# Kernel optimization log

Measured on AMD Instinct MI355X. Metric: run time of the kernel, lower is better.

Reference implementation:

```python
import jax, jax.numpy as jnp
import numpy as np

D_MODEL = 256
D_STATE = 256
BATCH = 32
SEQ = 4096
RMIN, RMAX = 0.9, 0.999
NEG_SLOPE = 0.01
EPS = 1e-5


def layer_norm(x, w=None, b=None):
    m = jnp.mean(x, axis=-1, keepdims=True)
    v = jnp.var(x, axis=-1, keepdims=True)
    y = (x - m) * jax.lax.rsqrt(v + EPS)
    if w is not None:
        y = y * w + b
    return y


def leaky_relu(x):
    return jnp.where(x >= 0, x, NEG_SLOPE * x)


def setup_inputs() -> dict:
    key = jax.random.key(0)
    ks = jax.random.split(key, 12)
    x = jax.random.normal(ks[0], (BATCH, SEQ, D_MODEL), dtype=jnp.float32)
    # LRU ring init: |lambda| uniform in [rmin, rmax], phase uniform in [0, 2pi]
    u1 = jax.random.uniform(ks[1], (D_STATE,), dtype=jnp.float32)
    u2 = jax.random.uniform(ks[2], (D_STATE,), dtype=jnp.float32)
    nu_log = jnp.log(-0.5 * jnp.log(u1 * (RMAX**2 - RMIN**2) + RMIN**2))
    theta_log = jnp.log(2 * jnp.pi * u2)
    lam_mod = jnp.exp(-jnp.exp(nu_log))
    gamma_log = jnp.log(jnp.sqrt(1.0 - lam_mod**2))
    B_re = jax.random.normal(ks[3], (D_STATE, D_MODEL)) / np.sqrt(2 * D_MODEL)
    B_im = jax.random.normal(ks[4], (D_STATE, D_MODEL)) / np.sqrt(2 * D_MODEL)
    C_re = jax.random.normal(ks[5], (D_STATE, D_STATE)) / np.sqrt(D_STATE)
    C_im = jax.random.normal(ks[6], (D_STATE, D_STATE)) / np.sqrt(D_STATE)
    Dm = jax.random.normal(ks[7], (D_STATE, D_MODEL)) / np.sqrt(D_MODEL)
    Wl = jax.random.normal(ks[8], (D_MODEL, D_STATE)) / np.sqrt(D_STATE)
    bl = jax.random.normal(ks[9], (D_MODEL,)) * 0.02
    Wr = jax.random.normal(ks[10], (D_MODEL, D_STATE)) / np.sqrt(D_STATE)
    br = jax.random.normal(ks[11], (D_MODEL,)) * 0.02
    ones_m = jnp.ones((D_MODEL,), jnp.float32)
    zeros_m = jnp.zeros((D_MODEL,), jnp.float32)
    ones_s = jnp.ones((D_STATE,), jnp.float32)
    zeros_s = jnp.zeros((D_STATE,), jnp.float32)
    return {
        "x": x,
        "ln1_w": ones_m, "ln1_b": zeros_m,
        "nu_log": nu_log, "theta_log": theta_log, "gamma_log": gamma_log,
        "B_re": B_re, "B_im": B_im, "C_re": C_re, "C_im": C_im, "Dm": Dm,
        "ln2_w": ones_s, "ln2_b": zeros_s,
        "Wl": Wl, "bl": bl, "Wr": Wr, "br": br,
        "ln4_w": ones_m, "ln4_b": zeros_m,
    }


def reference(x, ln1_w, ln1_b, nu_log, theta_log, gamma_log, B_re, B_im,
              C_re, C_im, Dm, ln2_w, ln2_b, Wl, bl, Wr, br, ln4_w, ln4_b):
    # pre-norm + residual skip
    x1 = layer_norm(x, ln1_w, ln1_b)          # [B, T, d_model]
    skip = x1
    u = leaky_relu(x1)
    # LRU: h_t = lambda * h_{t-1} + gamma * (B u_t); y = Re(C h) + D u
    lam_mod = jnp.exp(-jnp.exp(nu_log))
    theta = jnp.exp(theta_log)
    lr = lam_mod * jnp.cos(theta)             # [N]
    li = lam_mod * jnp.sin(theta)
    gam = jnp.exp(gamma_log)
    bu_re = gam * jnp.einsum('btd,nd->btn', u, B_re)  # [B, T, N]
    bu_im = gam * jnp.einsum('btd,nd->btn', u, B_im)
    bu_re_t = jnp.swapaxes(bu_re, 0, 1)       # [T, B, N]
    bu_im_t = jnp.swapaxes(bu_im, 0, 1)

    def step(carry, inp):
        hr, hi = carry
        br_t, bi_t = inp
        hr2 = lr * hr - li * hi + br_t
        hi2 = lr * hi + li * hr + bi_t
        return (hr2, hi2), (hr2, hi2)

    h0 = (jnp.zeros((x.shape[0], lr.shape[0]), x.dtype),
          jnp.zeros((x.shape[0], lr.shape[0]), x.dtype))
    (hr_last, hi_last), (hr, hi) = jax.lax.scan(step, h0, (bu_re_t, bu_im_t))
    hr = jnp.swapaxes(hr, 0, 1)               # [B, T, N]
    hi = jnp.swapaxes(hi, 0, 1)
    y = (jnp.einsum('btn,mn->btm', hr, C_re)
         - jnp.einsum('btn,mn->btm', hi, C_im)
         + jnp.einsum('btd,md->btm', u, Dm))  # [B, T, d_state]
    # post-norm + nonlinearity
    y = leaky_relu(layer_norm(y, ln2_w, ln2_b))
    # gated bilinear MLP
    xl = layer_norm(y @ Wl.T + bl)            # no affine
    xr = layer_norm(y @ Wr.T + br)
    out = layer_norm(xl * xr, ln4_w, ln4_b) + skip
    return out
```

## Files before the change

### kernel.cpp

```cpp
#include <hip/hip_runtime.h>
#include <cstdint>
#include <cstddef>

#define DEV __device__ __forceinline__

typedef unsigned short u16;
typedef short short8 __attribute__((ext_vector_type(8)));
typedef float floatx4 __attribute__((ext_vector_type(4)));

constexpr int BB = 32;
constexpr int TT = 4096;
constexpr int RR = BB * TT;
constexpr int CH = 64;
constexpr int LC = TT / CH;

constexpr size_t OFF_LAM  = 0;
constexpr size_t OFF_LAML = 2048;
constexpr size_t OFF_GAM  = 4096;
constexpr size_t OFF_B1   = 8192;
constexpr size_t OFF_B2   = OFF_B1 + (size_t)512 * 256 * 2;
constexpr size_t OFF_B3   = OFF_B2 + (size_t)256 * 768 * 2;
constexpr size_t OFF_BIG  = 2ull << 20;
constexpr size_t SZB      = (size_t)RR * 256 * 2;

DEV float bf2f(u16 u) {
    unsigned int i = ((unsigned int)u) << 16;
    float f;
    __builtin_memcpy(&f, &i, 4);
    return f;
}
DEV u16 f2bf(float f) {
    unsigned int i;
    __builtin_memcpy(&i, &f, 4);
    i += 0x7fffu + ((i >> 16) & 1u);
    return (u16)(i >> 16);
}

DEV void gload16(const void* g, void* l) {
    __builtin_amdgcn_global_load_lds(
        (const __attribute__((address_space(1))) unsigned int*)g,
        (__attribute__((address_space(3))) unsigned int*)l, 16, 0, 0);
}

__global__ __launch_bounds__(256)
void k_setup(const float* __restrict__ nu_log, const float* __restrict__ theta_log,
             const float* __restrict__ gamma_log,
             const float* __restrict__ B_re, const float* __restrict__ B_im,
             const float* __restrict__ C_re, const float* __restrict__ C_im,
             const float* __restrict__ Dm,
             const float* __restrict__ Wl, const float* __restrict__ Wr,
             char* __restrict__ ws)
{
    float2* lam  = (float2*)(ws + OFF_LAM);
    float2* lamL = (float2*)(ws + OFF_LAML);
    float*  gam  = (float*)(ws + OFF_GAM);
    u16* B1 = (u16*)(ws + OFF_B1);
    u16* B2 = (u16*)(ws + OFF_B2);
    u16* B3 = (u16*)(ws + OFF_B3);
    int g = blockIdx.x * 256 + threadIdx.x;
    int stride = gridDim.x * 256;
    if (g < 256) {
        float mod = expf(-expf(nu_log[g]));
        float th  = expf(theta_log[g]);
        float lr = mod * cosf(th), li = mod * sinf(th);
        lam[g] = make_float2(lr, li);
        gam[g] = expf(gamma_log[g]);
        float pr = 1.f, pi = 0.f;
        for (int i = 0; i < LC; i++) { float nr = pr*lr - pi*li; pi = pr*li + pi*lr; pr = nr; }
        lamL[g] = make_float2(pr, pi);
    }
    for (int i = g; i < 512*256; i += stride) {
        int n = i >> 8, d = i & 255;
        B1[i] = f2bf(n < 256 ? B_re[n*256 + d] : B_im[(n-256)*256 + d]);
    }
    for (int i = g; i < 256*768; i += stride) {
        int m = i / 768, k = i - m*768;
        float v = (k < 256) ? C_re[m*256 + k]
                : (k < 512) ? -C_im[m*256 + (k-256)]
                            : Dm[m*256 + (k-512)];
        B2[i] = f2bf(v);
    }
    for (int i = g; i < 512*256; i += stride) {
        int n = i >> 8, d = i & 255;
        B3[i] = f2bf(n < 256 ? Wl[n*256 + d] : Wr[(n-256)*256 + d]);
    }
}

__global__ __launch_bounds__(256)
void k_ln1(const float* __restrict__ x, const float* __restrict__ w, const float* __restrict__ b,
           u16* __restrict__ u, u16* __restrict__ skip)
{
    const int wv = threadIdx.x >> 6, lane = threadIdx.x & 63;
    const size_t row = (size_t)blockIdx.x * 4 + wv;
    float4 v = ((const float4*)(x + row * 256))[lane];
    float s = v.x + v.y + v.z + v.w;
    float q = v.x*v.x + v.y*v.y + v.z*v.z + v.w*v.w;
    #pragma unroll
    for (int o = 32; o; o >>= 1) { s += __shfl_xor(s, o); q += __shfl_xor(q, o); }
    const float m  = s * (1.f/256.f);
    const float rs = rsqrtf(q * (1.f/256.f) - m*m + 1e-5f);
    const float4 wv4 = ((const float4*)w)[lane];
    const float4 bv4 = ((const float4*)b)[lane];
    float y0 = (v.x - m) * rs * wv4.x + bv4.x;
    float y1 = (v.y - m) * rs * wv4.y + bv4.y;
    float y2 = (v.z - m) * rs * wv4.z + bv4.z;
    float y3 = (v.w - m) * rs * wv4.w + bv4.w;
    ((ushort4*)(skip + row * 256))[lane] = make_ushort4(f2bf(y0), f2bf(y1), f2bf(y2), f2bf(y3));
    float u0 = y0 >= 0.f ? y0 : 0.01f * y0;
    float u1 = y1 >= 0.f ? y1 : 0.01f * y1;
    float u2 = y2 >= 0.f ? y2 : 0.01f * y2;
    float u3 = y3 >= 0.f ? y3 : 0.01f * y3;
    ((ushort4*)(u + row * 256))[lane] = make_ushort4(f2bf(u0), f2bf(u1), f2bf(u2), f2bf(u3));
}

template<int MODE>
__global__ __launch_bounds__(256)
void k_gemm(const u16* __restrict__ A0, const u16* __restrict__ A1, const u16* __restrict__ A2,
            const u16* __restrict__ Bmat, u16* __restrict__ O0, u16* __restrict__ O1,
            const float* __restrict__ p0, const float* __restrict__ p1)
{
    constexpr int NKT = (MODE == 2) ? 12 : 4;
    constexpr int SB  = (MODE == 2) ? 768 : 256;
    __shared__ alignas(16) u16 As[2][128 * 64];
    __shared__ alignas(16) u16 Bs[2][128 * 64];
    const int wid = threadIdx.x >> 6, lane = threadIdx.x & 63;
    const int rowbase = blockIdx.x * 128;
    const int ct = blockIdx.y;
    const u16* Bbase = Bmat + (size_t)ct * 128 * SB;

    const int srow  = lane >> 3;
    const int sslot = (lane & 7) ^ srow;

    floatx4 acc[4][4];
    #pragma unroll
    for (int i = 0; i < 4; i++)
        #pragma unroll
        for (int j = 0; j < 4; j++)
            acc[i][j] = (floatx4){0.f, 0.f, 0.f, 0.f};

    auto stage = [&](int kt, int pb) {
        const u16* Asrc; int kofs;
        if (MODE == 2) {
            if (kt < 4)      { Asrc = A0; kofs = kt * 64; }
            else if (kt < 8) { Asrc = A1; kofs = (kt - 4) * 64; }
            else             { Asrc = A2; kofs = (kt - 8) * 64; }
        } else { Asrc = A0; kofs = kt * 64; }
        #pragma unroll
        for (int i = 0; i < 4; i++) {
            int grp = wid * 4 + i;
            int row = grp * 8 + srow;
            gload16(Asrc + (size_t)(rowbase + row) * 256 + kofs + sslot * 8,
                    (char*)&As[pb][0] + grp * 1024);
            gload16(Bbase + (size_t)row * SB + kt * 64 + sslot * 8,
                    (char*)&Bs[pb][0] + grp * 1024);
        }
    };

    stage(0, 0);
    const int wm = wid >> 1, wn = wid & 1;
    for (int kt = 0; kt < NKT; ++kt) {
        const int pb = kt & 1;
        if (kt + 1 < NKT) {
            stage(kt + 1, pb ^ 1);
            asm volatile("s_waitcnt vmcnt(8)" ::: "memory");
        } else {
            asm volatile("s_waitcnt vmcnt(0)" ::: "memory");
        }
        __builtin_amdgcn_s_barrier();
        short8 af[2][4], bfr[2][4];
        #pragma unroll
        for (int kk = 0; kk < 2; kk++) {
            const int rslot = (kk * 4 + (lane >> 4)) ^ (lane & 7);
            #pragma unroll
            for (int mi = 0; mi < 4; mi++)
                af[kk][mi] = *(const short8*)&As[pb][(wm*64 + mi*16 + (lane & 15)) * 64 + rslot * 8];
            #pragma unroll
            for (int ni = 0; ni < 4; ni++)
                bfr[kk][ni] = *(const short8*)&Bs[pb][(wn*64 + ni*16 + (lane & 15)) * 64 + rslot * 8];
        }
        #pragma unroll
        for (int mi = 0; mi < 4; mi++)
            #pragma unroll
            for (int ni = 0; ni < 4; ni++) {
                acc[mi][ni] = __builtin_amdgcn_mfma_f32_16x16x32_bf16(af[0][mi], bfr[0][ni], acc[mi][ni], 0, 0, 0);
                acc[mi][ni] = __builtin_amdgcn_mfma_f32_16x16x32_bf16(af[1][mi], bfr[1][ni], acc[mi][ni], 0, 0, 0);
            }
        __builtin_amdgcn_s_barrier();
    }

    #pragma unroll
    for (int mi = 0; mi < 4; mi++) {
        #pragma unroll
        for (int ni = 0; ni < 4; ni++) {
            const int cc = wn*64 + ni*16 + (lane & 15);
            const int n  = ct * 128 + cc;
            float scale = 1.f, badd = 0.f;
            u16* outp; int col;
            if (MODE == 1)      { outp = (n < 256) ? O0 : O1; col = n & 255; scale = p0[col]; }
            else if (MODE == 2) { outp = O0; col = n; }
            else                { outp = (n < 256) ? O0 : O1; col = n & 255; badd = (n < 256 ? p0 : p1)[col]; }
            #pragma unroll
            for (int r = 0; r < 4; r++) {
                const int row = rowbase + wm*64 + mi*16 + ((lane >> 4) << 2) + r;
                float v = acc[mi][ni][r] * scale + badd;
                outp[(size_t)row * 256 + col] = f2bf(v);
            }
        }
    }
}

__global__ __launch_bounds__(128)
void k_scan1(const u16* __restrict__ bre, const u16* __restrict__ bim,
             float4* __restrict__ carry, const char* __restrict__ ws)
{
    const float2* lam = (const float2*)(ws + OFF_LAM);
    const int b = blockIdx.x, c = blockIdx.y, p = threadIdx.x;
    const unsigned int* pre = (const unsigned int*)bre;
    const unsigned int* pim = (const unsigned int*)bim;
    const float2 l0 = lam[2*p], l1 = lam[2*p + 1];
    float hr0 = 0, hi0 = 0, hr1 = 0, hi1 = 0;
    size_t base = ((size_t)b * TT + (size_t)c * LC) * 128 + p;
    #pragma unroll 8
    for (int j = 0; j < LC; j++) {
        unsigned int re = pre[base + (size_t)j * 128];
        unsigned int im = pim[base + (size_t)j * 128];
        float br0 = bf2f((u16)(re & 0xffff)), br1 = bf2f((u16)(re >> 16));
        float bi0 = bf2f((u16)(im & 0xffff)), bi1 = bf2f((u16)(im >> 16));
        float nr0 = fmaf(l0.x, hr0, fmaf(-l0.y, hi0, br0));
        float ni0 = fmaf(l0.x, hi0, fmaf( l0.y, hr0, bi0));
        float nr1 = fmaf(l1.x, hr1, fmaf(-l1.y, hi1, br1));
        float ni1 = fmaf(l1.x, hi1, fmaf( l1.y, hr1, bi1));
        hr0 = nr0; hi0 = ni0; hr1 = nr1; hi1 = ni1;
    }
    carry[((size_t)b * CH + c) * 128 + p] = make_float4(hr0, hi0, hr1, hi1);
}

__global__ __launch_bounds__(128)
void k_comb(float4* __restrict__ carry, const char* __restrict__ ws)
{
    const float2* lamL = (const float2*)(ws + OFF_LAML);
    const int b = blockIdx.x, p = threadIdx.x;
    const float2 L0 = lamL[2*p], L1 = lamL[2*p + 1];
    float4 prev = make_float4(0.f, 0.f, 0.f, 0.f);
    size_t base = (size_t)b * CH * 128 + p;
    float4 nxt = carry[base];
    for (int c = 0; c < CH; c++) {
        float4 cur = nxt;
        if (c + 1 < CH) nxt = carry[base + (size_t)(c + 1) * 128];
        carry[base + (size_t)c * 128] = prev;
        float nx = fmaf(L0.x, prev.x, fmaf(-L0.y, prev.y, cur.x));
        float ny = fmaf(L0.x, prev.y, fmaf( L0.y, prev.x, cur.y));
        float nz = fmaf(L1.x, prev.z, fmaf(-L1.y, prev.w, cur.z));
        float nw = fmaf(L1.x, prev.w, fmaf( L1.y, prev.z, cur.w));
        prev = make_float4(nx, ny, nz, nw);
    }
}

__global__ __launch_bounds__(128)
void k_scan2(u16* __restrict__ bre, u16* __restrict__ bim,
             const float4* __restrict__ carry, const char* __restrict__ ws)
{
    const float2* lam = (const float2*)(ws + OFF_LAM);
    const int b = blockIdx.x, c = blockIdx.y, p = threadIdx.x;
    unsigned int* pre = (unsigned int*)bre;
    unsigned int* pim = (unsigned int*)bim;
    const float2 l0 = lam[2*p], l1 = lam[2*p + 1];
    float4 h0 = carry[((size_t)b * CH + c) * 128 + p];
    float hr0 = h0.x, hi0 = h0.y, hr1 = h0.z, hi1 = h0.w;
    size_t base = ((size_t)b * TT + (size_t)c * LC) * 128 + p;
    #pragma unroll 8
    for (int j = 0; j < LC; j++) {
        size_t idx = base + (size_t)j * 128;
        unsigned int re = pre[idx];
        unsigned int im = pim[idx];
        float br0 = bf2f((u16)(re & 0xffff)), br1 = bf2f((u16)(re >> 16));
        float bi0 = bf2f((u16)(im & 0xffff)), bi1 = bf2f((u16)(im >> 16));
        float nr0 = fmaf(l0.x, hr0, fmaf(-l0.y, hi0, br0));
        float ni0 = fmaf(l0.x, hi0, fmaf( l0.y, hr0, bi0));
        float nr1 = fmaf(l1.x, hr1, fmaf(-l1.y, hi1, br1));
        float ni1 = fmaf(l1.x, hi1, fmaf( l1.y, hr1, bi1));
        hr0 = nr0; hi0 = ni0; hr1 = nr1; hi1 = ni1;
        pre[idx] = ((unsigned int)f2bf(hr1) << 16) | f2bf(hr0);
        pim[idx] = ((unsigned int)f2bf(hi1) << 16) | f2bf(hi0);
    }
}

__global__ __launch_bounds__(256)
void k_ln2(u16* __restrict__ y, const float* __restrict__ w, const float* __restrict__ b)
{
    const int wv = threadIdx.x >> 6, lane = threadIdx.x & 63;
    const size_t row = (size_t)blockIdx.x * 4 + wv;
    ushort4 raw = ((const ushort4*)(y + row * 256))[lane];
    float v0 = bf2f(raw.x), v1 = bf2f(raw.y), v2 = bf2f(raw.z), v3 = bf2f(raw.w);
    float s = v0 + v1 + v2 + v3;
    float q = v0*v0 + v1*v1 + v2*v2 + v3*v3;
    #pragma unroll
    for (int o = 32; o; o >>= 1) { s += __shfl_xor(s, o); q += __shfl_xor(q, o); }
    const float m  = s * (1.f/256.f);
    const float rs = rsqrtf(q * (1.f/256.f) - m*m + 1e-5f);
    const float4 wv4 = ((const float4*)w)[lane];
    const float4 bv4 = ((const float4*)b)[lane];
    float y0 = (v0 - m) * rs * wv4.x + bv4.x;
    float y1 = (v1 - m) * rs * wv4.y + bv4.y;
    float y2 = (v2 - m) * rs * wv4.z + bv4.z;
    float y3 = (v3 - m) * rs * wv4.w + bv4.w;
    y0 = y0 >= 0.f ? y0 : 0.01f * y0;
    y1 = y1 >= 0.f ? y1 : 0.01f * y1;
    y2 = y2 >= 0.f ? y2 : 0.01f * y2;
    y3 = y3 >= 0.f ? y3 : 0.01f * y3;
    ((ushort4*)(y + row * 256))[lane] = make_ushort4(f2bf(y0), f2bf(y1), f2bf(y2), f2bf(y3));
}

__global__ __launch_bounds__(256)
void k_final(const u16* __restrict__ gl, const u16* __restrict__ gr, const u16* __restrict__ skip,
             const float* __restrict__ w4, const float* __restrict__ b4, float* __restrict__ out)
{
    const int wv = threadIdx.x >> 6, lane = threadIdx.x & 63;
    const size_t row = (size_t)blockIdx.x * 4 + wv;
    ushort4 ra = ((const ushort4*)(gl + row * 256))[lane];
    ushort4 rc = ((const ushort4*)(gr + row * 256))[lane];
    float a0 = bf2f(ra.x), a1 = bf2f(ra.y), a2 = bf2f(ra.z), a3 = bf2f(ra.w);
    float c0 = bf2f(rc.x), c1 = bf2f(rc.y), c2 = bf2f(rc.z), c3 = bf2f(rc.w);
    float s1 = a0+a1+a2+a3, q1 = a0*a0+a1*a1+a2*a2+a3*a3;
    float s2 = c0+c1+c2+c3, q2 = c0*c0+c1*c1+c2*c2+c3*c3;
    #pragma unroll
    for (int o = 32; o; o >>= 1) {
        s1 += __shfl_xor(s1, o); q1 += __shfl_xor(q1, o);
        s2 += __shfl_xor(s2, o); q2 += __shfl_xor(q2, o);
    }
    const float m1 = s1*(1.f/256.f), rs1 = rsqrtf(q1*(1.f/256.f) - m1*m1 + 1e-5f);
    const float m2 = s2*(1.f/256.f), rs2 = rsqrtf(q2*(1.f/256.f) - m2*m2 + 1e-5f);
    float v0 = ((a0-m1)*rs1) * ((c0-m2)*rs2);
    float v1 = ((a1-m1)*rs1) * ((c1-m2)*rs2);
    float v2 = ((a2-m1)*rs1) * ((c2-m2)*rs2);
    float v3 = ((a3-m1)*rs1) * ((c3-m2)*rs2);
    float s3 = v0+v1+v2+v3, q3 = v0*v0+v1*v1+v2*v2+v3*v3;
    #pragma unroll
    for (int o = 32; o; o >>= 1) { s3 += __shfl_xor(s3, o); q3 += __shfl_xor(q3, o); }
    const float m3 = s3*(1.f/256.f), rs3 = rsqrtf(q3*(1.f/256.f) - m3*m3 + 1e-5f);
    const float4 wv4 = ((const float4*)w4)[lane];
    const float4 bv4 = ((const float4*)b4)[lane];
    ushort4 sk = ((const ushort4*)(skip + row * 256))[lane];
    float o0 = (v0-m3)*rs3*wv4.x + bv4.x + bf2f(sk.x);
    float o1 = (v1-m3)*rs3*wv4.y + bv4.y + bf2f(sk.y);
    float o2 = (v2-m3)*rs3*wv4.z + bv4.z + bf2f(sk.z);
    float o3 = (v3-m3)*rs3*wv4.w + bv4.w + bf2f(sk.w);
    ((float4*)(out + row * 256))[lane] = make_float4(o0, o1, o2, o3);
}

extern "C" void kernel_launch(void* const* d_in, const int* in_sizes, int n_in,
                              void* d_out, int out_size, void* d_ws, size_t ws_size,
                              hipStream_t stream)
{
    (void)in_sizes; (void)n_in; (void)out_size; (void)ws_size;
    const float* x         = (const float*)d_in[0];
    const float* ln1_w     = (const float*)d_in[1];
    const float* ln1_b     = (const float*)d_in[2];
    const float* nu_log    = (const float*)d_in[3];
    const float* theta_log = (const float*)d_in[4];
    const float* gamma_log = (const float*)d_in[5];
    const float* B_re      = (const float*)d_in[6];
    const float* B_im      = (const float*)d_in[7];
    const float* C_re      = (const float*)d_in[8];
    const float* C_im      = (const float*)d_in[9];
    const float* Dm        = (const float*)d_in[10];
    const float* ln2_w     = (const float*)d_in[11];
    const float* ln2_b     = (const float*)d_in[12];
    const float* Wl        = (const float*)d_in[13];
    const float* bl        = (const float*)d_in[14];
    const float* Wr        = (const float*)d_in[15];
    const float* br        = (const float*)d_in[16];
    const float* ln4_w     = (const float*)d_in[17];
    const float* ln4_b     = (const float*)d_in[18];

    char* ws = (char*)d_ws;
    float* gam = (float*)(ws + OFF_GAM);
    u16* B1 = (u16*)(ws + OFF_B1);
    u16* B2 = (u16*)(ws + OFF_B2);
    u16* B3 = (u16*)(ws + OFF_B3);
    u16* u    = (u16*)(ws + OFF_BIG);
    u16* skip = (u16*)(ws + OFF_BIG + 1 * SZB);
    u16* bure = (u16*)(ws + OFF_BIG + 2 * SZB);
    u16* buim = (u16*)(ws + OFF_BIG + 3 * SZB);
    u16* y    = (u16*)(ws + OFF_BIG + 4 * SZB);
    float4* carry = (float4*)(ws + OFF_BIG + 5 * SZB);
    float* out = (float*)d_out;

    k_setup<<<dim3(256), dim3(256), 0, stream>>>(nu_log, theta_log, gamma_log,
                                                 B_re, B_im, C_re, C_im, Dm, Wl, Wr, ws);
    k_ln1<<<dim3(RR/4), dim3(256), 0, stream>>>(x, ln1_w, ln1_b, u, skip);
    k_gemm<1><<<dim3(RR/128, 4), dim3(256), 0, stream>>>(u, nullptr, nullptr, B1, bure, buim, gam, nullptr);
    k_scan1<<<dim3(BB, CH), dim3(128), 0, stream>>>(bure, buim, carry, ws);
    k_comb<<<dim3(BB), dim3(128), 0, stream>>>(carry, ws);
    k_scan2<<<dim3(BB, CH), dim3(128), 0, stream>>>(bure, buim, carry, ws);
    k_gemm<2><<<dim3(RR/128, 2), dim3(256), 0, stream>>>(bure, buim, u, B2, y, nullptr, nullptr, nullptr);
    k_ln2<<<dim3(RR/4), dim3(256), 0, stream>>>(y, ln2_w, ln2_b);
    k_gemm<3><<<dim3(RR/128, 4), dim3(256), 0, stream>>>(y, nullptr, nullptr, B3, bure, buim, bl, br);
    k_final<<<dim3(RR/4), dim3(256), 0, stream>>>(bure, buim, skip, ln4_w, ln4_b, out);
}
```

Baseline: 438.7 us.

## Fuse LayerNorm epilogues into full-row GEMM2 and GEMM3 kernels

GEMM2 now computes all 256 output columns per block with 8 waves, so the LN2 and leaky-ReLU epilogue can run in-register with cross-wave row statistics in shared memory, and the separate ln2 kernel goes away. GEMM3 computes both 256-column halves per 64-row block and applies the two row LayerNorms, the gating product, the final LayerNorm and the skip add in the epilogue, which removes k_final and the bf16 round trip of xl and xr. The aim is to cut global memory traffic and launches. In exchange it uses 512-thread blocks with large shared memory, 32-wide K steps and unswizzled LDS tiles that may cause bank conflicts, and GEMM3 stages A with 4-byte loads.

```diff
diff --git a/kernel.cpp b/kernel.cpp
--- a/kernel.cpp
+++ b/kernel.cpp
@@ -40,6 +40,11 @@
     __builtin_amdgcn_global_load_lds(
         (const __attribute__((address_space(1))) unsigned int*)g,
         (__attribute__((address_space(3))) unsigned int*)l, 16, 0, 0);
+}
+DEV void gload4(const void* g, void* l) {
+    __builtin_amdgcn_global_load_lds(
+        (const __attribute__((address_space(1))) unsigned int*)g,
+        (__attribute__((address_space(3))) unsigned int*)l, 4, 0, 0);
 }
 
 __global__ __launch_bounds__(256)
@@ -113,54 +118,38 @@
     ((ushort4*)(u + row * 256))[lane] = make_ushort4(f2bf(u0), f2bf(u1), f2bf(u2), f2bf(u3));
 }
 
-template<int MODE>
 __global__ __launch_bounds__(256)
-void k_gemm(const u16* __restrict__ A0, const u16* __restrict__ A1, const u16* __restrict__ A2,
-            const u16* __restrict__ Bmat, u16* __restrict__ O0, u16* __restrict__ O1,
-            const float* __restrict__ p0, const float* __restrict__ p1)
-{
-    constexpr int NKT = (MODE == 2) ? 12 : 4;
-    constexpr int SB  = (MODE == 2) ? 768 : 256;
+void k_gemm1(const u16* __restrict__ A0, const u16* __restrict__ Bmat,
+             u16* __restrict__ O0, u16* __restrict__ O1, const float* __restrict__ p0)
+{
     __shared__ alignas(16) u16 As[2][128 * 64];
     __shared__ alignas(16) u16 Bs[2][128 * 64];
     const int wid = threadIdx.x >> 6, lane = threadIdx.x & 63;
     const int rowbase = blockIdx.x * 128;
     const int ct = blockIdx.y;
-    const u16* Bbase = Bmat + (size_t)ct * 128 * SB;
-
+    const u16* Bbase = Bmat + (size_t)ct * 128 * 256;
     const int srow  = lane >> 3;
     const int sslot = (lane & 7) ^ srow;
-
-    floatx4 acc[4][4];
-    #pragma unroll
-    for (int i = 0; i < 4; i++)
-        #pragma unroll
-        for (int j = 0; j < 4; j++)
-            acc[i][j] = (floatx4){0.f, 0.f, 0.f, 0.f};
+    floatx4 acc[4][4] = {};
 
     auto stage = [&](int kt, int pb) {
-        const u16* Asrc; int kofs;
-        if (MODE == 2) {
-            if (kt < 4)      { Asrc = A0; kofs = kt * 64; }
-            else if (kt < 8) { Asrc = A1; kofs = (kt - 4) * 64; }
-            else             { Asrc = A2; kofs = (kt - 8) * 64; }
-        } else { Asrc = A0; kofs = kt * 64; }
+        int kofs = kt * 64;
         #pragma unroll
         for (int i = 0; i < 4; i++) {
             int grp = wid * 4 + i;
             int row = grp * 8 + srow;
-            gload16(Asrc + (size_t)(rowbase + row) * 256 + kofs + sslot * 8,
+            gload16(A0 + (size_t)(rowbase + row) * 256 + kofs + sslot * 8,
                     (char*)&As[pb][0] + grp * 1024);
-            gload16(Bbase + (size_t)row * SB + kt * 64 + sslot * 8,
+            gload16(Bbase + (size_t)row * 256 + kofs + sslot * 8,
                     (char*)&Bs[pb][0] + grp * 1024);
         }
     };
 
     stage(0, 0);
     const int wm = wid >> 1, wn = wid & 1;
-    for (int kt = 0; kt < NKT; ++kt) {
+    for (int kt = 0; kt < 4; ++kt) {
         const int pb = kt & 1;
-        if (kt + 1 < NKT) {
+        if (kt + 1 < 4) {
             stage(kt + 1, pb ^ 1);
             asm volatile("s_waitcnt vmcnt(8)" ::: "memory");
         } else {
@@ -187,25 +176,336 @@
             }
         __builtin_amdgcn_s_barrier();
     }
-
     #pragma unroll
     for (int mi = 0; mi < 4; mi++) {
         #pragma unroll
         for (int ni = 0; ni < 4; ni++) {
             const int cc = wn*64 + ni*16 + (lane & 15);
             const int n  = ct * 128 + cc;
-            float scale = 1.f, badd = 0.f;
-            u16* outp; int col;
-            if (MODE == 1)      { outp = (n < 256) ? O0 : O1; col = n & 255; scale = p0[col]; }
-            else if (MODE == 2) { outp = O0; col = n; }
-            else                { outp = (n < 256) ? O0 : O1; col = n & 255; badd = (n < 256 ? p0 : p1)[col]; }
+            u16* outp = (n < 256) ? O0 : O1;
+            const int col = n & 255;
+            const float scale = p0[col];
             #pragma unroll
             for (int r = 0; r < 4; r++) {
                 const int row = rowbase + wm*64 + mi*16 + ((lane >> 4) << 2) + r;
-                float v = acc[mi][ni][r] * scale + badd;
-                outp[(size_t)row * 256 + col] = f2bf(v);
-            }
-        }
+                outp[(size_t)row * 256 + col] = f2bf(acc[mi][ni][r] * scale);
+            }
+        }
+    }
+}
+
+__global__ __launch_bounds__(512)
+void k_gemm2(const u16* __restrict__ Ahr, const u16* __restrict__ Ahi, const u16* __restrict__ Au,
+             const u16* __restrict__ Bm, u16* __restrict__ Oy,
+             const float* __restrict__ w2, const float* __restrict__ b2)
+{
+    __shared__ alignas(16) char smem[49152 + 4096];
+    u16*   As0 = (u16*)smem;
+    u16*   Bs0 = (u16*)(smem + 16384);
+    float* st  = (float*)(smem + 49152);
+    const int tid = threadIdx.x, wid = tid >> 6, lane = tid & 63;
+    const int lanelo = lane & 15, lanehi = lane >> 4;
+    const int rowbase = blockIdx.x * 128;
+    const int wm = wid >> 2, wn = wid & 3;
+    floatx4 acc[4][4] = {};
+
+    auto stage = [&](int kt, int pb) {
+        const u16* Asrc = (kt < 8) ? Ahr : (kt < 16) ? Ahi : Au;
+        const int kofs = (kt & 7) * 32;
+        { int g = tid; int row = g >> 2, slot = g & 3;
+          gload16(Asrc + (size_t)(rowbase + row) * 256 + kofs + slot * 8,
+                  (char*)(As0 + pb * 4096) + (wid * 64) * 16); }
+        #pragma unroll
+        for (int j = 0; j < 2; j++) {
+            int g = j * 512 + tid; int row = g >> 2, slot = g & 3;
+            gload16(Bm + (size_t)row * 768 + kt * 32 + slot * 8,
+                    (char*)(Bs0 + pb * 8192) + (j * 512 + wid * 64) * 16);
+        }
+    };
+
+    stage(0, 0);
+    for (int kt = 0; kt < 24; ++kt) {
+        const int pb = kt & 1;
+        if (kt + 1 < 24) {
+            stage(kt + 1, pb ^ 1);
+            asm volatile("s_waitcnt vmcnt(3)" ::: "memory");
+        } else {
+            asm volatile("s_waitcnt vmcnt(0)" ::: "memory");
+        }
+        __builtin_amdgcn_s_barrier();
+        short8 af[4], bfr[4];
+        #pragma unroll
+        for (int mi = 0; mi < 4; mi++)
+            af[mi] = *(const short8*)&As0[pb*4096 + (wm*64 + mi*16 + lanelo)*32 + lanehi*8];
+        #pragma unroll
+        for (int ni = 0; ni < 4; ni++)
+            bfr[ni] = *(const short8*)&Bs0[pb*8192 + (wn*64 + ni*16 + lanelo)*32 + lanehi*8];
+        #pragma unroll
+        for (int mi = 0; mi < 4; mi++)
+            #pragma unroll
+            for (int ni = 0; ni < 4; ni++)
+                acc[mi][ni] = __builtin_amdgcn_mfma_f32_16x16x32_bf16(af[mi], bfr[ni], acc[mi][ni], 0, 0, 0);
+        __builtin_amdgcn_s_barrier();
+    }
+
+    float sarr[4][4], qarr[4][4];
+    #pragma unroll
+    for (int mi = 0; mi < 4; mi++)
+        #pragma unroll
+        for (int r = 0; r < 4; r++) {
+            float s = 0.f, q = 0.f;
+            #pragma unroll
+            for (int ni = 0; ni < 4; ni++) { float v = acc[mi][ni][r]; s += v; q += v*v; }
+            sarr[mi][r] = s; qarr[mi][r] = q;
+        }
+    #pragma unroll
+    for (int o = 1; o < 16; o <<= 1)
+        #pragma unroll
+        for (int mi = 0; mi < 4; mi++)
+            #pragma unroll
+            for (int r = 0; r < 4; r++) {
+                sarr[mi][r] += __shfl_xor(sarr[mi][r], o);
+                qarr[mi][r] += __shfl_xor(qarr[mi][r], o);
+            }
+    if (lanelo == 0) {
+        #pragma unroll
+        for (int mi = 0; mi < 4; mi++)
+            #pragma unroll
+            for (int r = 0; r < 4; r++) {
+                int rw = mi*16 + lanehi*4 + r;
+                st[(wid*64 + rw)*2 + 0] = sarr[mi][r];
+                st[(wid*64 + rw)*2 + 1] = qarr[mi][r];
+            }
+    }
+    __syncthreads();
+    float wc[4], bc[4];
+    #pragma unroll
+    for (int ni = 0; ni < 4; ni++) {
+        int col = wn*64 + ni*16 + lanelo;
+        wc[ni] = w2[col]; bc[ni] = b2[col];
+    }
+    #pragma unroll
+    for (int mi = 0; mi < 4; mi++)
+        #pragma unroll
+        for (int r = 0; r < 4; r++) {
+            const int rw = mi*16 + lanehi*4 + r;
+            float S = 0.f, Q = 0.f;
+            #pragma unroll
+            for (int ww = 0; ww < 4; ww++) {
+                S += st[((wm*4 + ww)*64 + rw)*2 + 0];
+                Q += st[((wm*4 + ww)*64 + rw)*2 + 1];
+            }
+            const float m  = S * (1.f/256.f);
+            const float rs = rsqrtf(Q * (1.f/256.f) - m*m + 1e-5f);
+            const size_t row = (size_t)rowbase + wm*64 + rw;
+            #pragma unroll
+            for (int ni = 0; ni < 4; ni++) {
+                int col = wn*64 + ni*16 + lanelo;
+                float v = (acc[mi][ni][r] - m) * rs * wc[ni] + bc[ni];
+                v = v >= 0.f ? v : 0.01f * v;
+                Oy[row * 256 + col] = f2bf(v);
+            }
+        }
+}
+
+__global__ __launch_bounds__(512)
+void k_gemm3f(const u16* __restrict__ Ay, const u16* __restrict__ Bm,
+              const float* __restrict__ bl, const float* __restrict__ brr,
+              const float* __restrict__ w4, const float* __restrict__ b4,
+              const u16* __restrict__ skip, float* __restrict__ out)
+{
+    __shared__ alignas(16) char smem[73728];
+    u16*   As0 = (u16*)smem;
+    u16*   Bs0 = (u16*)(smem + 8192);
+    float* xrb = (float*)smem;
+    float* st  = (float*)(smem + 65536);
+    float* st4 = (float*)(smem + 65536 + 4096);
+    const int tid = threadIdx.x, wid = tid >> 6, lane = tid & 63;
+    const int lanelo = lane & 15, lanehi = lane >> 4;
+    const int rowbase = blockIdx.x * 64;
+    const int wn = wid;
+    floatx4 acc[4][4] = {};
+
+    auto stage = [&](int kt, int pb) {
+        const int kofs = kt * 32;
+        #pragma unroll
+        for (int j = 0; j < 2; j++) {
+            int d = j * 512 + tid; int row = d >> 4, dc = d & 15;
+            gload4(Ay + (size_t)(rowbase + row) * 256 + kofs + dc * 2,
+                   (char*)(As0 + pb * 2048) + (j * 512 + wid * 64) * 4);
+        }
+        #pragma unroll
+        for (int j = 0; j < 4; j++) {
+            int g = j * 512 + tid; int row = g >> 2, slot = g & 3;
+            gload16(Bm + (size_t)row * 256 + kofs + slot * 8,
+                    (char*)(Bs0 + pb * 16384) + (j * 512 + wid * 64) * 16);
+        }
+    };
+
+    stage(0, 0);
+    for (int kt = 0; kt < 8; ++kt) {
+        const int pb = kt & 1;
+        if (kt + 1 < 8) {
+            stage(kt + 1, pb ^ 1);
+            asm volatile("s_waitcnt vmcnt(6)" ::: "memory");
+        } else {
+            asm volatile("s_waitcnt vmcnt(0)" ::: "memory");
+        }
+        __builtin_amdgcn_s_barrier();
+        short8 af[4], bfr[4];
+        #pragma unroll
+        for (int mi = 0; mi < 4; mi++)
+            af[mi] = *(const short8*)&As0[pb*2048 + (mi*16 + lanelo)*32 + lanehi*8];
+        #pragma unroll
+        for (int ni = 0; ni < 4; ni++)
+            bfr[ni] = *(const short8*)&Bs0[pb*16384 + (wn*64 + ni*16 + lanelo)*32 + lanehi*8];
+        #pragma unroll
+        for (int mi = 0; mi < 4; mi++)
+            #pragma unroll
+            for (int ni = 0; ni < 4; ni++)
+                acc[mi][ni] = __builtin_amdgcn_mfma_f32_16x16x32_bf16(af[mi], bfr[ni], acc[mi][ni], 0, 0, 0);
+        __builtin_amdgcn_s_barrier();
+    }
+
+    float bc[4];
+    #pragma unroll
+    for (int ni = 0; ni < 4; ni++) {
+        int col = wn*64 + ni*16 + lanelo;
+        bc[ni] = (col < 256) ? bl[col] : brr[col - 256];
+    }
+    #pragma unroll
+    for (int mi = 0; mi < 4; mi++)
+        #pragma unroll
+        for (int ni = 0; ni < 4; ni++)
+            #pragma unroll
+            for (int r = 0; r < 4; r++)
+                acc[mi][ni][r] += bc[ni];
+    float sarr[4][4], qarr[4][4];
+    #pragma unroll
+    for (int mi = 0; mi < 4; mi++)
+        #pragma unroll
+        for (int r = 0; r < 4; r++) {
+            float s = 0.f, q = 0.f;
+            #pragma unroll
+            for (int ni = 0; ni < 4; ni++) { float v = acc[mi][ni][r]; s += v; q += v*v; }
+            sarr[mi][r] = s; qarr[mi][r] = q;
+        }
+    #pragma unroll
+    for (int o = 1; o < 16; o <<= 1)
+        #pragma unroll
+        for (int mi = 0; mi < 4; mi++)
+            #pragma unroll
+            for (int r = 0; r < 4; r++) {
+                sarr[mi][r] += __shfl_xor(sarr[mi][r], o);
+                qarr[mi][r] += __shfl_xor(qarr[mi][r], o);
+            }
+    __syncthreads();
+    if (lanelo == 0) {
+        #pragma unroll
+        for (int mi = 0; mi < 4; mi++)
+            #pragma unroll
+            for (int r = 0; r < 4; r++) {
+                int rw = mi*16 + lanehi*4 + r;
+                st[(wid*64 + rw)*2 + 0] = sarr[mi][r];
+                st[(wid*64 + rw)*2 + 1] = qarr[mi][r];
+            }
+    }
+    __syncthreads();
+    const int half = wn >> 2;
+    #pragma unroll
+    for (int mi = 0; mi < 4; mi++)
+        #pragma unroll
+        for (int r = 0; r < 4; r++) {
+            const int rw = mi*16 + lanehi*4 + r;
+            float S = 0.f, Q = 0.f;
+            #pragma unroll
+            for (int ww = 0; ww < 4; ww++) {
+                S += st[((half*4 + ww)*64 + rw)*2 + 0];
+                Q += st[((half*4 + ww)*64 + rw)*2 + 1];
+            }
+            const float m  = S * (1.f/256.f);
+            const float rs = rsqrtf(Q * (1.f/256.f) - m*m + 1e-5f);
+            #pragma unroll
+            for (int ni = 0; ni < 4; ni++)
+                acc[mi][ni][r] = (acc[mi][ni][r] - m) * rs;
+        }
+    if (half) {
+        #pragma unroll
+        for (int mi = 0; mi < 4; mi++)
+            #pragma unroll
+            for (int r = 0; r < 4; r++) {
+                const int rw = mi*16 + lanehi*4 + r;
+                #pragma unroll
+                for (int ni = 0; ni < 4; ni++)
+                    xrb[rw*256 + (wn - 4)*64 + ni*16 + lanelo] = acc[mi][ni][r];
+            }
+    }
+    __syncthreads();
+    if (!half) {
+        #pragma unroll
+        for (int mi = 0; mi < 4; mi++)
+            #pragma unroll
+            for (int r = 0; r < 4; r++) {
+                const int rw = mi*16 + lanehi*4 + r;
+                float s = 0.f, q = 0.f;
+                #pragma unroll
+                for (int ni = 0; ni < 4; ni++) {
+                    float p = acc[mi][ni][r] * xrb[rw*256 + wn*64 + ni*16 + lanelo];
+                    acc[mi][ni][r] = p;
+                    s += p; q += p*p;
+                }
+                sarr[mi][r] = s; qarr[mi][r] = q;
+            }
+        #pragma unroll
+        for (int o = 1; o < 16; o <<= 1)
+            #pragma unroll
+            for (int mi = 0; mi < 4; mi++)
+                #pragma unroll
+                for (int r = 0; r < 4; r++) {
+                    sarr[mi][r] += __shfl_xor(sarr[mi][r], o);
+                    qarr[mi][r] += __shfl_xor(qarr[mi][r], o);
+                }
+        if (lanelo == 0) {
+            #pragma unroll
+            for (int mi = 0; mi < 4; mi++)
+                #pragma unroll
+                for (int r = 0; r < 4; r++) {
+                    int rw = mi*16 + lanehi*4 + r;
+                    st4[(wn*64 + rw)*2 + 0] = sarr[mi][r];
+                    st4[(wn*64 + rw)*2 + 1] = qarr[mi][r];
+                }
+        }
+    }
+    __syncthreads();
+    if (!half) {
+        float w4c[4], b4c[4];
+        #pragma unroll
+        for (int ni = 0; ni < 4; ni++) {
+            int col = wn*64 + ni*16 + lanelo;
+            w4c[ni] = w4[col]; b4c[ni] = b4[col];
+        }
+        #pragma unroll
+        for (int mi = 0; mi < 4; mi++)
+            #pragma unroll
+            for (int r = 0; r < 4; r++) {
+                const int rw = mi*16 + lanehi*4 + r;
+                float S = 0.f, Q = 0.f;
+                #pragma unroll
+                for (int ww = 0; ww < 4; ww++) {
+                    S += st4[(ww*64 + rw)*2 + 0];
+                    Q += st4[(ww*64 + rw)*2 + 1];
+                }
+                const float m  = S * (1.f/256.f);
+                const float rs = rsqrtf(Q * (1.f/256.f) - m*m + 1e-5f);
+                const size_t row = (size_t)rowbase + rw;
+                #pragma unroll
+                for (int ni = 0; ni < 4; ni++) {
+                    int col = wn*64 + ni*16 + lanelo;
+                    float o = (acc[mi][ni][r] - m) * rs * w4c[ni] + b4c[ni]
+                            + bf2f(skip[row*256 + col]);
+                    out[row*256 + col] = o;
+                }
+            }
     }
 }
 
@@ -285,69 +585,6 @@
     }
 }
 
-__global__ __launch_bounds__(256)
-void k_ln2(u16* __restrict__ y, const float* __restrict__ w, const float* __restrict__ b)
-{
-    const int wv = threadIdx.x >> 6, lane = threadIdx.x & 63;
-    const size_t row = (size_t)blockIdx.x * 4 + wv;
-    ushort4 raw = ((const ushort4*)(y + row * 256))[lane];
-    float v0 = bf2f(raw.x), v1 = bf2f(raw.y), v2 = bf2f(raw.z), v3 = bf2f(raw.w);
-    float s = v0 + v1 + v2 + v3;
-    float q = v0*v0 + v1*v1 + v2*v2 + v3*v3;
-    #pragma unroll
-    for (int o = 32; o; o >>= 1) { s += __shfl_xor(s, o); q += __shfl_xor(q, o); }
-    const float m  = s * (1.f/256.f);
-    const float rs = rsqrtf(q * (1.f/256.f) - m*m + 1e-5f);
-    const float4 wv4 = ((const float4*)w)[lane];
-    const float4 bv4 = ((const float4*)b)[lane];
-    float y0 = (v0 - m) * rs * wv4.x + bv4.x;
-    float y1 = (v1 - m) * rs * wv4.y + bv4.y;
-    float y2 = (v2 - m) * rs * wv4.z + bv4.z;
-    float y3 = (v3 - m) * rs * wv4.w + bv4.w;
-    y0 = y0 >= 0.f ? y0 : 0.01f * y0;
-    y1 = y1 >= 0.f ? y1 : 0.01f * y1;
-    y2 = y2 >= 0.f ? y2 : 0.01f * y2;
-    y3 = y3 >= 0.f ? y3 : 0.01f * y3;
-    ((ushort4*)(y + row * 256))[lane] = make_ushort4(f2bf(y0), f2bf(y1), f2bf(y2), f2bf(y3));
-}
-
-__global__ __launch_bounds__(256)
-void k_final(const u16* __restrict__ gl, const u16* __restrict__ gr, const u16* __restrict__ skip,
-             const float* __restrict__ w4, const float* __restrict__ b4, float* __restrict__ out)
-{
-    const int wv = threadIdx.x >> 6, lane = threadIdx.x & 63;
-    const size_t row = (size_t)blockIdx.x * 4 + wv;
-    ushort4 ra = ((const ushort4*)(gl + row * 256))[lane];
-    ushort4 rc = ((const ushort4*)(gr + row * 256))[lane];
-    float a0 = bf2f(ra.x), a1 = bf2f(ra.y), a2 = bf2f(ra.z), a3 = bf2f(ra.w);
-    float c0 = bf2f(rc.x), c1 = bf2f(rc.y), c2 = bf2f(rc.z), c3 = bf2f(rc.w);
-    float s1 = a0+a1+a2+a3, q1 = a0*a0+a1*a1+a2*a2+a3*a3;
-    float s2 = c0+c1+c2+c3, q2 = c0*c0+c1*c1+c2*c2+c3*c3;
-    #pragma unroll
-    for (int o = 32; o; o >>= 1) {
-        s1 += __shfl_xor(s1, o); q1 += __shfl_xor(q1, o);
-        s2 += __shfl_xor(s2, o); q2 += __shfl_xor(q2, o);
-    }
-    const float m1 = s1*(1.f/256.f), rs1 = rsqrtf(q1*(1.f/256.f) - m1*m1 + 1e-5f);
-    const float m2 = s2*(1.f/256.f), rs2 = rsqrtf(q2*(1.f/256.f) - m2*m2 + 1e-5f);
-    float v0 = ((a0-m1)*rs1) * ((c0-m2)*rs2);
-    float v1 = ((a1-m1)*rs1) * ((c1-m2)*rs2);
-    float v2 = ((a2-m1)*rs1) * ((c2-m2)*rs2);
-    float v3 = ((a3-m1)*rs1) * ((c3-m2)*rs2);
-    float s3 = v0+v1+v2+v3, q3 = v0*v0+v1*v1+v2*v2+v3*v3;
-    #pragma unroll
-    for (int o = 32; o; o >>= 1) { s3 += __shfl_xor(s3, o); q3 += __shfl_xor(q3, o); }
-    const float m3 = s3*(1.f/256.f), rs3 = rsqrtf(q3*(1.f/256.f) - m3*m3 + 1e-5f);
-    const float4 wv4 = ((const float4*)w4)[lane];
-    const float4 bv4 = ((const float4*)b4)[lane];
-    ushort4 sk = ((const ushort4*)(skip + row * 256))[lane];
-    float o0 = (v0-m3)*rs3*wv4.x + bv4.x + bf2f(sk.x);
-    float o1 = (v1-m3)*rs3*wv4.y + bv4.y + bf2f(sk.y);
-    float o2 = (v2-m3)*rs3*wv4.z + bv4.z + bf2f(sk.z);
-    float o3 = (v3-m3)*rs3*wv4.w + bv4.w + bf2f(sk.w);
-    ((float4*)(out + row * 256))[lane] = make_float4(o0, o1, o2, o3);
-}
-
 extern "C" void kernel_launch(void* const* d_in, const int* in_sizes, int n_in,
                               void* d_out, int out_size, void* d_ws, size_t ws_size,
                               hipStream_t stream)
@@ -389,12 +626,10 @@
     k_setup<<<dim3(256), dim3(256), 0, stream>>>(nu_log, theta_log, gamma_log,
                                                  B_re, B_im, C_re, C_im, Dm, Wl, Wr, ws);
     k_ln1<<<dim3(RR/4), dim3(256), 0, stream>>>(x, ln1_w, ln1_b, u, skip);
-    k_gemm<1><<<dim3(RR/128, 4), dim3(256), 0, stream>>>(u, nullptr, nullptr, B1, bure, buim, gam, nullptr);
+    k_gemm1<<<dim3(RR/128, 4), dim3(256), 0, stream>>>(u, B1, bure, buim, gam);
     k_scan1<<<dim3(BB, CH), dim3(128), 0, stream>>>(bure, buim, carry, ws);
     k_comb<<<dim3(BB), dim3(128), 0, stream>>>(carry, ws);
     k_scan2<<<dim3(BB, CH), dim3(128), 0, stream>>>(bure, buim, carry, ws);
-    k_gemm<2><<<dim3(RR/128, 2), dim3(256), 0, stream>>>(bure, buim, u, B2, y, nullptr, nullptr, nullptr);
-    k_ln2<<<dim3(RR/4), dim3(256), 0, stream>>>(y, ln2_w, ln2_b);
-    k_gemm<3><<<dim3(RR/128, 4), dim3(256), 0, stream>>>(y, nullptr, nullptr, B3, bure, buim, bl, br);
-    k_final<<<dim3(RR/4), dim3(256), 0, stream>>>(bure, buim, skip, ln4_w, ln4_b, out);
-}
+    k_gemm2<<<dim3(RR/128), dim3(512), 0, stream>>>(bure, buim, u, B2, y, ln2_w, ln2_b);
+    k_gemm3f<<<dim3(RR/64), dim3(512), 0, stream>>>(y, B3, bl, br, ln4_w, ln4_b, skip, out);
+}
```

Result: slower. 477.8 us (+8.9%).
